# Optimization experiments

Measured on AMD Instinct MI355X. Metric: run time of the kernel, lower is better.

The kernel has to match this reference:

```python
import jax, jax.numpy as jnp
import numpy as np

TOPK = 2


def setup_inputs() -> dict:
    key = jax.random.key(0)
    k1, k2, k3, k4, k5 = jax.random.split(key, 5)
    D, H, E = 1024, 1408, 8
    hidden_states = jax.random.normal(k1, (2, 1024, D), dtype=jnp.float32)
    gate_w = jax.random.normal(k2, (E, D), dtype=jnp.float32) * 0.02
    w1g = jax.random.normal(k3, (E, D, H), dtype=jnp.float32) * 0.02
    w1u = jax.random.normal(k4, (E, D, H), dtype=jnp.float32) * 0.02
    w2 = jax.random.normal(k5, (E, H, D), dtype=jnp.float32) * 0.02
    return {"hidden_states": hidden_states, "gate_w": gate_w, "w1g": w1g, "w1u": w1u, "w2": w2}


def reference(hidden_states, gate_w, w1g, w1u, w2):
    # hidden_states: [B, S, D]; expert weights: w1g/w1u [E, D, H], w2 [E, H, D]
    B, S, D = hidden_states.shape
    E = gate_w.shape[0]
    x = hidden_states.reshape(-1, D)  # [T, D]
    T = x.shape[0]

    # --- MoEGate: softmax scores, top-k routing (no topk renorm) ---
    logits = x @ gate_w.T                      # [T, E]
    scores = jax.nn.softmax(logits, axis=-1)   # [T, E]
    topk_w, topk_idx = jax.lax.top_k(scores, TOPK)  # [T, K]

    # Per-token combine coefficient for each expert: coeff[t, e] = sum_k w[t,k] * (idx[t,k]==e)
    coeff = jnp.zeros((T, E), dtype=x.dtype).at[jnp.arange(T)[:, None], topk_idx].add(topk_w)

    # --- Grouped expert MLP (swiglu): identical math to permute + grouped GEMM + unpermute ---
    g = jnp.einsum('td,edh->teh', x, w1g)      # [T, E, H]
    u = jnp.einsum('td,edh->teh', x, w1u)      # [T, E, H]
    h = jax.nn.silu(g) * u                     # [T, E, H]
    y = jnp.einsum('teh,te,ehd->td', h, coeff, w2)  # [T, D]
    return y.reshape(B, S, D)
```

## Files before the change

### kernel.cpp

```cpp
#include <hip/hip_runtime.h>

#define TOK 2048
#define DDIM 1024
#define HDIM 1408
#define ENUM 8
#define NSLOT (2 * TOK)
#define UP_NB 22
#define UP_KS 32
#define DN_NB 16
#define DN_KS 44

typedef unsigned int uint;
typedef unsigned short ushort;

using bf16x8 = __attribute__((ext_vector_type(8))) __bf16;
using f32x4  = __attribute__((ext_vector_type(4))) float;

__device__ __forceinline__ float silu_f(float g) {
    return g / (1.0f + __expf(-g));
}

__device__ __forceinline__ ushort cvt_bf16(float f) {
    uint u = __float_as_uint(f);
    u += 0x7FFFu + ((u >> 16) & 1u);
    return (ushort)(u >> 16);
}

__device__ __forceinline__ void gl2lds16(const void* g, void* l) {
    __builtin_amdgcn_global_load_lds(
        (const __attribute__((address_space(1))) uint*)g,
        (__attribute__((address_space(3))) uint*)l, 16, 0, 0);
}

__global__ __launch_bounds__(64) void gate1_kernel(
    const float* __restrict__ x, const float* __restrict__ gw,
    int* __restrict__ tinfo, float* __restrict__ wslot, ushort* __restrict__ xb)
{
    const int t = blockIdx.x;
    const int lane = threadIdx.x;
    const float* xr = x + (size_t)t * DDIM;
    ushort* xbr = xb + (size_t)t * DDIM;
    float xv[16];
#pragma unroll
    for (int i = 0; i < 16; ++i) xv[i] = xr[lane + 64 * i];
#pragma unroll
    for (int i = 0; i < 16; ++i) xbr[lane + 64 * i] = cvt_bf16(xv[i]);
    float logit[ENUM];
#pragma unroll
    for (int e = 0; e < ENUM; ++e) {
        const float* gr = gw + (size_t)e * DDIM;
        float acc = 0.f;
#pragma unroll
        for (int i = 0; i < 16; ++i) acc += xv[i] * gr[lane + 64 * i];
#pragma unroll
        for (int s = 32; s > 0; s >>= 1) acc += __shfl_xor(acc, s, 64);
        logit[e] = acc;
    }
    if (lane == 0) {
        float mx = logit[0];
#pragma unroll
        for (int e = 1; e < ENUM; ++e) mx = fmaxf(mx, logit[e]);
        float p[ENUM]; float se = 0.f;
#pragma unroll
        for (int e = 0; e < ENUM; ++e) { p[e] = __expf(logit[e] - mx); se += p[e]; }
        float inv = 1.0f / se;
#pragma unroll
        for (int e = 0; e < ENUM; ++e) p[e] *= inv;
        int i0 = 0;
#pragma unroll
        for (int e = 1; e < ENUM; ++e) if (p[e] > p[i0]) i0 = e;
        int i1 = (i0 == 0) ? 1 : 0;
#pragma unroll
        for (int e = 0; e < ENUM; ++e) if (e != i0 && p[e] > p[i1]) i1 = e;
        tinfo[t] = i0 | (i1 << 4);
        wslot[(t << 1)] = p[i0];
        wslot[(t << 1) | 1] = p[i1];
    }
}

__global__ __launch_bounds__(256) void gate2_kernel(
    const int* __restrict__ tinfo, int* __restrict__ counts, int* __restrict__ toks)
{
    __shared__ int cnt[ENUM];
    const int tid = threadIdx.x;
    if (tid < ENUM) cnt[tid] = 0;
    __syncthreads();
    for (int t = tid; t < TOK; t += 256) {
        int info = tinfo[t];
        int i0 = info & 15, i1 = info >> 4;
        int p0 = atomicAdd(&cnt[i0], 1);
        toks[i0 * TOK + p0] = (t << 1);
        int p1 = atomicAdd(&cnt[i1], 1);
        toks[i1 * TOK + p1] = (t << 1) | 1;
    }
    __syncthreads();
    if (tid < ENUM) counts[tid] = cnt[tid];
}

__device__ __forceinline__ void tcast64_body(
    const float* __restrict__ src, ushort* __restrict__ dst, int N, int KS, int NB,
    int e, int ks, int nb, int tid)
{
    __shared__ float Ls[32][68];
    const float* st = src + (size_t)e * ((size_t)KS * 32) * N + (size_t)(ks * 32) * N + nb * 64;
    const int n4 = (tid & 15) * 4;
#pragma unroll
    for (int r = 0; r < 2; ++r) {
        int k = (tid >> 4) + r * 16;
        float4 v = *(const float4*)(st + (size_t)k * N + n4);
        Ls[k][n4 + 0] = v.x; Ls[k][n4 + 1] = v.y; Ls[k][n4 + 2] = v.z; Ls[k][n4 + 3] = v.w;
    }
    __syncthreads();

    ushort* dt = dst + ((((size_t)e * NB + nb) * KS) + ks) * 2048;
    const int nn = tid >> 2;
    const int kk0 = (tid & 3) * 8;
    ushort o[8];
#pragma unroll
    for (int j = 0; j < 8; ++j) o[j] = cvt_bf16(Ls[kk0 + j][nn]);
    *(uint4*)(dt + nn * 32 + kk0) = *(uint4*)o;
}

__global__ __launch_bounds__(256) void tcast_w1_kernel(
    const float* __restrict__ w1g, const float* __restrict__ w1u,
    ushort* __restrict__ BgP, ushort* __restrict__ BuP)
{
    const int z = blockIdx.z;
    const float* src = (z & 8) ? w1u : w1g;
    ushort* dst = (z & 8) ? BuP : BgP;
    tcast64_body(src, dst, HDIM, UP_KS, UP_NB, z & 7, blockIdx.x, blockIdx.y, threadIdx.x);
}

__global__ __launch_bounds__(256) void tcast_w2_kernel(
    const float* __restrict__ w2, ushort* __restrict__ W2P)
{
    tcast64_body(w2, W2P, DDIM, DN_KS, DN_NB, blockIdx.z, blockIdx.x, blockIdx.y, threadIdx.x);
}

__global__ __launch_bounds__(256, 4) void up_mfma(
    const ushort* __restrict__ xb, const ushort* __restrict__ BgP,
    const ushort* __restrict__ BuP, const int* __restrict__ counts,
    const int* __restrict__ toks, ushort* __restrict__ Hbuf)
{
    const int e = blockIdx.z;
    const int cnt = counts[e];
    const int m0 = blockIdx.y * 64;
    if (m0 >= cnt) return;
    const int nb = blockIdx.x;
    const int tid = threadIdx.x;
    const int w = tid >> 6;
    const int lane = tid & 63;
    const int q = lane >> 4;
    const int l15 = lane & 15;
    const int wr = w >> 1;
    const int wc = w & 1;

    __shared__ ushort As[2][64][32];
    __shared__ ushort Bgs[2][64][32];
    __shared__ ushort Bus[2][64][32];
    __shared__ int rowslot[64];

    if (tid < 64) rowslot[tid] = (m0 + tid < cnt) ? toks[e * TOK + m0 + tid] : -1;
    __syncthreads();

    const int srow = w * 16 + (lane >> 2);
    const int clog = (((lane & 3) + 4 - ((srow >> 1) & 3)) & 3) * 8;
    const int aslot = rowslot[srow];
    const ushort* agp = xb + (size_t)(aslot < 0 ? 0 : (aslot >> 1)) * DDIM + clog;
    const size_t tb = (size_t)(e * UP_NB + nb) * UP_KS * 2048;
    const ushort* bgp = BgP + tb + srow * 32 + clog;
    const ushort* bup = BuP + tb + srow * 32 + clog;

    const int coff = ((q + (l15 >> 1)) & 3) * 8;

    f32x4 accg[2][2], accu[2][2];
#pragma unroll
    for (int i = 0; i < 2; ++i)
#pragma unroll
        for (int j = 0; j < 2; ++j) { accg[i][j] = (f32x4)0.f; accu[i][j] = (f32x4)0.f; }

#define UP_PREFETCH(KSV, B)                                       \
    {                                                             \
        gl2lds16(agp + (KSV) * 32, &As[B][w * 16][0]);            \
        gl2lds16(bgp + (size_t)(KSV) * 2048, &Bgs[B][w * 16][0]); \
        gl2lds16(bup + (size_t)(KSV) * 2048, &Bus[B][w * 16][0]); \
    }

    UP_PREFETCH(0, 0);
    __syncthreads();

    for (int ks = 0; ks < UP_KS; ++ks) {
        const int cur = ks & 1;
        const int nxt = cur ^ 1;
        if (ks + 1 < UP_KS) UP_PREFETCH(ks + 1, nxt);

        bf16x8 a[2], bg[2], bu[2];
#pragma unroll
        for (int mi = 0; mi < 2; ++mi)
            a[mi] = *(const bf16x8*)&As[cur][wr * 32 + mi * 16 + l15][coff];
#pragma unroll
        for (int ni = 0; ni < 2; ++ni) {
            bg[ni] = *(const bf16x8*)&Bgs[cur][wc * 32 + ni * 16 + l15][coff];
            bu[ni] = *(const bf16x8*)&Bus[cur][wc * 32 + ni * 16 + l15][coff];
        }
#pragma unroll
        for (int mi = 0; mi < 2; ++mi)
#pragma unroll
            for (int ni = 0; ni < 2; ++ni) {
                accg[mi][ni] = __builtin_amdgcn_mfma_f32_16x16x32_bf16(a[mi], bg[ni], accg[mi][ni], 0, 0, 0);
                accu[mi][ni] = __builtin_amdgcn_mfma_f32_16x16x32_bf16(a[mi], bu[ni], accu[mi][ni], 0, 0, 0);
            }
        __syncthreads();
    }
#undef UP_PREFETCH

#pragma unroll
    for (int mi = 0; mi < 2; ++mi) {
#pragma unroll
        for (int r = 0; r < 4; ++r) {
            int ml = wr * 32 + mi * 16 + q * 4 + r;
            int slot = rowslot[ml];
            if (slot < 0) continue;
            ushort* hrow = Hbuf + (size_t)slot * HDIM + nb * 64 + wc * 32 + l15;
#pragma unroll
            for (int ni = 0; ni < 2; ++ni)
                hrow[ni * 16] = cvt_bf16(silu_f(accg[mi][ni][r]) * accu[mi][ni][r]);
        }
    }
}

__global__ __launch_bounds__(256, 4) void down_mfma(
    const ushort* __restrict__ Hbuf, const ushort* __restrict__ W2P,
    const int* __restrict__ counts, const int* __restrict__ toks,
    float* __restrict__ Ybuf)
{
    const int e = blockIdx.z;
    const int cnt = counts[e];
    const int m0 = blockIdx.y * 64;
    if (m0 >= cnt) return;
    const int nb = blockIdx.x;
    const int tid = threadIdx.x;
    const int w = tid >> 6;
    const int lane = tid & 63;
    const int q = lane >> 4;
    const int l15 = lane & 15;
    const int wr = w >> 1;
    const int wc = w & 1;

    __shared__ ushort As[2][64][32];
    __shared__ ushort Bs[2][64][32];
    __shared__ int rowslot[64];

    if (tid < 64) rowslot[tid] = (m0 + tid < cnt) ? toks[e * TOK + m0 + tid] : -1;
    __syncthreads();

    const int srow = w * 16 + (lane >> 2);
    const int clog = (((lane & 3) + 4 - ((srow >> 1) & 3)) & 3) * 8;
    const int aslot = rowslot[srow];
    const ushort* agp = Hbuf + (size_t)(aslot < 0 ? 0 : aslot) * HDIM + clog;
    const ushort* bp = W2P + (size_t)(e * DN_NB + nb) * DN_KS * 2048 + srow * 32 + clog;

    const int coff = ((q + (l15 >> 1)) & 3) * 8;

    f32x4 acc[2][2];
#pragma unroll
    for (int i = 0; i < 2; ++i)
#pragma unroll
        for (int j = 0; j < 2; ++j) acc[i][j] = (f32x4)0.f;

#define DN_PREFETCH(KSV, B)                                     \
    {                                                           \
        gl2lds16(agp + (KSV) * 32, &As[B][w * 16][0]);          \
        gl2lds16(bp + (size_t)(KSV) * 2048, &Bs[B][w * 16][0]); \
    }

    DN_PREFETCH(0, 0);
    __syncthreads();

    for (int ks = 0; ks < DN_KS; ++ks) {
        const int cur = ks & 1;
        const int nxt = cur ^ 1;
        if (ks + 1 < DN_KS) DN_PREFETCH(ks + 1, nxt);

        bf16x8 a[2], b[2];
#pragma unroll
        for (int mi = 0; mi < 2; ++mi)
            a[mi] = *(const bf16x8*)&As[cur][wr * 32 + mi * 16 + l15][coff];
#pragma unroll
        for (int ni = 0; ni < 2; ++ni)
            b[ni] = *(const bf16x8*)&Bs[cur][wc * 32 + ni * 16 + l15][coff];
#pragma unroll
        for (int mi = 0; mi < 2; ++mi)
#pragma unroll
            for (int ni = 0; ni < 2; ++ni)
                acc[mi][ni] = __builtin_amdgcn_mfma_f32_16x16x32_bf16(a[mi], b[ni], acc[mi][ni], 0, 0, 0);
        __syncthreads();
    }
#undef DN_PREFETCH

#pragma unroll
    for (int mi = 0; mi < 2; ++mi) {
#pragma unroll
        for (int r = 0; r < 4; ++r) {
            int ml = wr * 32 + mi * 16 + q * 4 + r;
            int slot = rowslot[ml];
            if (slot < 0) continue;
            float* yr = Ybuf + (size_t)slot * DDIM + nb * 64 + wc * 32 + l15;
#pragma unroll
            for (int ni = 0; ni < 2; ++ni)
                yr[ni * 16] = acc[mi][ni][r];
        }
    }
}

__global__ __launch_bounds__(256) void combine_kernel(
    const float* __restrict__ Ybuf, const float* __restrict__ wslot,
    float* __restrict__ y)
{
    const int t = blockIdx.x;
    const int j = threadIdx.x * 4;
    const float w0 = wslot[2 * t];
    const float w1 = wslot[2 * t + 1];
    float4 a = *(const float4*)(Ybuf + ((size_t)2 * t) * DDIM + j);
    float4 b = *(const float4*)(Ybuf + ((size_t)2 * t + 1) * DDIM + j);
    float4 o;
    o.x = w0 * a.x + w1 * b.x;
    o.y = w0 * a.y + w1 * b.y;
    o.z = w0 * a.z + w1 * b.z;
    o.w = w0 * a.w + w1 * b.w;
    *(float4*)(y + (size_t)t * DDIM + j) = o;
}

extern "C" void kernel_launch(void* const* d_in, const int* in_sizes, int n_in,
                              void* d_out, int out_size, void* d_ws, size_t ws_size,
                              hipStream_t stream) {
    const float* x   = (const float*)d_in[0];
    const float* gw  = (const float*)d_in[1];
    const float* w1g = (const float*)d_in[2];
    const float* w1u = (const float*)d_in[3];
    const float* w2  = (const float*)d_in[4];
    float* y = (float*)d_out;
    char* ws = (char*)d_ws;

    size_t off = 0;
    int*    counts = (int*)(ws + off);   off += 256;
    int*    toks   = (int*)(ws + off);   off += (size_t)ENUM * TOK * 4;
    float*  wslot  = (float*)(ws + off); off += (size_t)NSLOT * 4;
    int*    tinfo  = (int*)(ws + off);   off += (size_t)TOK * 4;
    off = (off + 255) & ~(size_t)255;
    ushort* xb     = (ushort*)(ws + off); off += (size_t)TOK * DDIM * 2;
    size_t regA = off;
    ushort* BgP  = (ushort*)(ws + regA);
    ushort* BuP  = (ushort*)(ws + regA + (size_t)ENUM * DDIM * HDIM * 2);
    float*  Ybuf = (float*)(ws + regA);
    off = regA + (size_t)2 * ENUM * DDIM * HDIM * 2;
    ushort* W2P  = (ushort*)(ws + off);  off += (size_t)ENUM * HDIM * DDIM * 2;
    ushort* Hbuf = (ushort*)(ws + off);

    gate1_kernel<<<TOK, 64, 0, stream>>>(x, gw, tinfo, wslot, xb);
    gate2_kernel<<<1, 256, 0, stream>>>(tinfo, counts, toks);

    tcast_w1_kernel<<<dim3(UP_KS, UP_NB, 16), 256, 0, stream>>>(w1g, w1u, BgP, BuP);
    tcast_w2_kernel<<<dim3(DN_KS, DN_NB, ENUM), 256, 0, stream>>>(w2, W2P);

    up_mfma<<<dim3(UP_NB, TOK / 64, ENUM), 256, 0, stream>>>(xb, BgP, BuP, counts, toks, Hbuf);
    down_mfma<<<dim3(DN_NB, TOK / 64, ENUM), 256, 0, stream>>>(Hbuf, W2P, counts, toks, Ybuf);
    combine_kernel<<<TOK, 256, 0, stream>>>(Ybuf, wslot, y);
}
```

Before: 272.0 us.

## Enlarge expert GEMM block tiles from 64x64 to 128x128

Doubles the M and N tile of both grouped expert GEMMs to 128x128, so each wave computes a 64x64 sub-tile with 4x4 MFMA fragments. The weight pre-cast kernels now write 128-column packed panels to match the new layout. Each staged A and B tile feeds more MFMAs, which lowers global and LDS traffic per FLOP. The cost is many more accumulator registers (launch bounds lowered to 2 blocks per SM) and more padded work on expert tiles that are only partly filled.

After: 278.2 us. 1.02x slower.

```diff
diff --git a/kernel.cpp b/kernel.cpp
--- a/kernel.cpp
+++ b/kernel.cpp
@@ -5,9 +5,9 @@
 #define HDIM 1408
 #define ENUM 8
 #define NSLOT (2 * TOK)
-#define UP_NB 22
+#define UP_NB 11
 #define UP_KS 32
-#define DN_NB 16
+#define DN_NB 8
 #define DN_KS 44
 
 typedef unsigned int uint;
@@ -97,28 +97,29 @@
     if (tid < ENUM) counts[tid] = cnt[tid];
 }
 
-__device__ __forceinline__ void tcast64_body(
+__device__ __forceinline__ void tcast128_body(
     const float* __restrict__ src, ushort* __restrict__ dst, int N, int KS, int NB,
     int e, int ks, int nb, int tid)
 {
-    __shared__ float Ls[32][68];
-    const float* st = src + (size_t)e * ((size_t)KS * 32) * N + (size_t)(ks * 32) * N + nb * 64;
-    const int n4 = (tid & 15) * 4;
-#pragma unroll
-    for (int r = 0; r < 2; ++r) {
-        int k = (tid >> 4) + r * 16;
+    __shared__ float Ls[32][132];
+    const float* st = src + (size_t)e * ((size_t)KS * 32) * N + (size_t)(ks * 32) * N + nb * 128;
+    const int n4 = (tid & 31) * 4;
+#pragma unroll
+    for (int r = 0; r < 4; ++r) {
+        int k = (tid >> 5) + r * 8;
         float4 v = *(const float4*)(st + (size_t)k * N + n4);
         Ls[k][n4 + 0] = v.x; Ls[k][n4 + 1] = v.y; Ls[k][n4 + 2] = v.z; Ls[k][n4 + 3] = v.w;
     }
     __syncthreads();
 
-    ushort* dt = dst + ((((size_t)e * NB + nb) * KS) + ks) * 2048;
-    const int nn = tid >> 2;
-    const int kk0 = (tid & 3) * 8;
-    ushort o[8];
-#pragma unroll
-    for (int j = 0; j < 8; ++j) o[j] = cvt_bf16(Ls[kk0 + j][nn]);
-    *(uint4*)(dt + nn * 32 + kk0) = *(uint4*)o;
+    ushort* dt = dst + ((((size_t)e * NB + nb) * KS) + ks) * 4096;
+    const int nn = tid >> 1;
+    const int kk0 = (tid & 1) * 16;
+    ushort o[16];
+#pragma unroll
+    for (int j = 0; j < 16; ++j) o[j] = cvt_bf16(Ls[kk0 + j][nn]);
+    *(uint4*)(dt + nn * 32 + kk0)     = *(uint4*)&o[0];
+    *(uint4*)(dt + nn * 32 + kk0 + 8) = *(uint4*)&o[8];
 }
 
 __global__ __launch_bounds__(256) void tcast_w1_kernel(
@@ -128,23 +129,23 @@
     const int z = blockIdx.z;
     const float* src = (z & 8) ? w1u : w1g;
     ushort* dst = (z & 8) ? BuP : BgP;
-    tcast64_body(src, dst, HDIM, UP_KS, UP_NB, z & 7, blockIdx.x, blockIdx.y, threadIdx.x);
+    tcast128_body(src, dst, HDIM, UP_KS, UP_NB, z & 7, blockIdx.x, blockIdx.y, threadIdx.x);
 }
 
 __global__ __launch_bounds__(256) void tcast_w2_kernel(
     const float* __restrict__ w2, ushort* __restrict__ W2P)
 {
-    tcast64_body(w2, W2P, DDIM, DN_KS, DN_NB, blockIdx.z, blockIdx.x, blockIdx.y, threadIdx.x);
-}
-
-__global__ __launch_bounds__(256, 4) void up_mfma(
+    tcast128_body(w2, W2P, DDIM, DN_KS, DN_NB, blockIdx.z, blockIdx.x, blockIdx.y, threadIdx.x);
+}
+
+__global__ __launch_bounds__(256, 2) void up_mfma(
     const ushort* __restrict__ xb, const ushort* __restrict__ BgP,
     const ushort* __restrict__ BuP, const int* __restrict__ counts,
     const int* __restrict__ toks, ushort* __restrict__ Hbuf)
 {
     const int e = blockIdx.z;
     const int cnt = counts[e];
-    const int m0 = blockIdx.y * 64;
+    const int m0 = blockIdx.y * 128;
     if (m0 >= cnt) return;
     const int nb = blockIdx.x;
     const int tid = threadIdx.x;
@@ -155,35 +156,41 @@
     const int wr = w >> 1;
     const int wc = w & 1;
 
-    __shared__ ushort As[2][64][32];
-    __shared__ ushort Bgs[2][64][32];
-    __shared__ ushort Bus[2][64][32];
-    __shared__ int rowslot[64];
-
-    if (tid < 64) rowslot[tid] = (m0 + tid < cnt) ? toks[e * TOK + m0 + tid] : -1;
-    __syncthreads();
-
-    const int srow = w * 16 + (lane >> 2);
-    const int clog = (((lane & 3) + 4 - ((srow >> 1) & 3)) & 3) * 8;
-    const int aslot = rowslot[srow];
-    const ushort* agp = xb + (size_t)(aslot < 0 ? 0 : (aslot >> 1)) * DDIM + clog;
-    const size_t tb = (size_t)(e * UP_NB + nb) * UP_KS * 2048;
-    const ushort* bgp = BgP + tb + srow * 32 + clog;
-    const ushort* bup = BuP + tb + srow * 32 + clog;
+    __shared__ ushort As[2][128][32];
+    __shared__ ushort Bgs[2][128][32];
+    __shared__ ushort Bus[2][128][32];
+    __shared__ int rowslot[128];
+
+    if (tid < 128) rowslot[tid] = (m0 + tid < cnt) ? toks[e * TOK + m0 + tid] : -1;
+    __syncthreads();
+
+    const int srow0 = w * 32 + (lane >> 2);
+    const int srow1 = srow0 + 16;
+    const int clog = (((lane & 3) + 4 - ((srow0 >> 1) & 3)) & 3) * 8;
+    const int s0 = rowslot[srow0];
+    const int s1 = rowslot[srow1];
+    const ushort* agp0 = xb + (size_t)(s0 < 0 ? 0 : (s0 >> 1)) * DDIM + clog;
+    const ushort* agp1 = xb + (size_t)(s1 < 0 ? 0 : (s1 >> 1)) * DDIM + clog;
+    const size_t tb = (size_t)(e * UP_NB + nb) * UP_KS * 4096;
+    const ushort* bgp = BgP + tb + srow0 * 32 + clog;
+    const ushort* bup = BuP + tb + srow0 * 32 + clog;
 
     const int coff = ((q + (l15 >> 1)) & 3) * 8;
 
-    f32x4 accg[2][2], accu[2][2];
-#pragma unroll
-    for (int i = 0; i < 2; ++i)
-#pragma unroll
-        for (int j = 0; j < 2; ++j) { accg[i][j] = (f32x4)0.f; accu[i][j] = (f32x4)0.f; }
-
-#define UP_PREFETCH(KSV, B)                                       \
-    {                                                             \
-        gl2lds16(agp + (KSV) * 32, &As[B][w * 16][0]);            \
-        gl2lds16(bgp + (size_t)(KSV) * 2048, &Bgs[B][w * 16][0]); \
-        gl2lds16(bup + (size_t)(KSV) * 2048, &Bus[B][w * 16][0]); \
+    f32x4 accg[4][4], accu[4][4];
+#pragma unroll
+    for (int i = 0; i < 4; ++i)
+#pragma unroll
+        for (int j = 0; j < 4; ++j) { accg[i][j] = (f32x4)0.f; accu[i][j] = (f32x4)0.f; }
+
+#define UP_PREFETCH(KSV, B)                                                 \
+    {                                                                       \
+        gl2lds16(agp0 + (KSV) * 32, &As[B][w * 32][0]);                     \
+        gl2lds16(agp1 + (KSV) * 32, &As[B][w * 32 + 16][0]);                \
+        gl2lds16(bgp + (size_t)(KSV) * 4096, &Bgs[B][w * 32][0]);           \
+        gl2lds16(bgp + (size_t)(KSV) * 4096 + 512, &Bgs[B][w * 32 + 16][0]);\
+        gl2lds16(bup + (size_t)(KSV) * 4096, &Bus[B][w * 32][0]);           \
+        gl2lds16(bup + (size_t)(KSV) * 4096 + 512, &Bus[B][w * 32 + 16][0]);\
     }
 
     UP_PREFETCH(0, 0);
@@ -194,19 +201,19 @@
         const int nxt = cur ^ 1;
         if (ks + 1 < UP_KS) UP_PREFETCH(ks + 1, nxt);
 
-        bf16x8 a[2], bg[2], bu[2];
-#pragma unroll
-        for (int mi = 0; mi < 2; ++mi)
-            a[mi] = *(const bf16x8*)&As[cur][wr * 32 + mi * 16 + l15][coff];
-#pragma unroll
-        for (int ni = 0; ni < 2; ++ni) {
-            bg[ni] = *(const bf16x8*)&Bgs[cur][wc * 32 + ni * 16 + l15][coff];
-            bu[ni] = *(const bf16x8*)&Bus[cur][wc * 32 + ni * 16 + l15][coff];
+        bf16x8 a[4], bg[4], bu[4];
+#pragma unroll
+        for (int mi = 0; mi < 4; ++mi)
+            a[mi] = *(const bf16x8*)&As[cur][wr * 64 + mi * 16 + l15][coff];
+#pragma unroll
+        for (int ni = 0; ni < 4; ++ni) {
+            bg[ni] = *(const bf16x8*)&Bgs[cur][wc * 64 + ni * 16 + l15][coff];
+            bu[ni] = *(const bf16x8*)&Bus[cur][wc * 64 + ni * 16 + l15][coff];
         }
 #pragma unroll
-        for (int mi = 0; mi < 2; ++mi)
-#pragma unroll
-            for (int ni = 0; ni < 2; ++ni) {
+        for (int mi = 0; mi < 4; ++mi)
+#pragma unroll
+            for (int ni = 0; ni < 4; ++ni) {
                 accg[mi][ni] = __builtin_amdgcn_mfma_f32_16x16x32_bf16(a[mi], bg[ni], accg[mi][ni], 0, 0, 0);
                 accu[mi][ni] = __builtin_amdgcn_mfma_f32_16x16x32_bf16(a[mi], bu[ni], accu[mi][ni], 0, 0, 0);
             }
@@ -215,28 +222,28 @@
 #undef UP_PREFETCH
 
 #pragma unroll
-    for (int mi = 0; mi < 2; ++mi) {
+    for (int mi = 0; mi < 4; ++mi) {
 #pragma unroll
         for (int r = 0; r < 4; ++r) {
-            int ml = wr * 32 + mi * 16 + q * 4 + r;
+            int ml = wr * 64 + mi * 16 + q * 4 + r;
             int slot = rowslot[ml];
             if (slot < 0) continue;
-            ushort* hrow = Hbuf + (size_t)slot * HDIM + nb * 64 + wc * 32 + l15;
-#pragma unroll
-            for (int ni = 0; ni < 2; ++ni)
+            ushort* hrow = Hbuf + (size_t)slot * HDIM + nb * 128 + wc * 64 + l15;
+#pragma unroll
+            for (int ni = 0; ni < 4; ++ni)
                 hrow[ni * 16] = cvt_bf16(silu_f(accg[mi][ni][r]) * accu[mi][ni][r]);
         }
     }
 }
 
-__global__ __launch_bounds__(256, 4) void down_mfma(
+__global__ __launch_bounds__(256, 2) void down_mfma(
     const ushort* __restrict__ Hbuf, const ushort* __restrict__ W2P,
     const int* __restrict__ counts, const int* __restrict__ toks,
     float* __restrict__ Ybuf)
 {
     const int e = blockIdx.z;
     const int cnt = counts[e];
-    const int m0 = blockIdx.y * 64;
+    const int m0 = blockIdx.y * 128;
     if (m0 >= cnt) return;
     const int nb = blockIdx.x;
     const int tid = threadIdx.x;
@@ -247,31 +254,36 @@
     const int wr = w >> 1;
     const int wc = w & 1;
 
-    __shared__ ushort As[2][64][32];
-    __shared__ ushort Bs[2][64][32];
-    __shared__ int rowslot[64];
-
-    if (tid < 64) rowslot[tid] = (m0 + tid < cnt) ? toks[e * TOK + m0 + tid] : -1;
-    __syncthreads();
-
-    const int srow = w * 16 + (lane >> 2);
-    const int clog = (((lane & 3) + 4 - ((srow >> 1) & 3)) & 3) * 8;
-    const int aslot = rowslot[srow];
-    const ushort* agp = Hbuf + (size_t)(aslot < 0 ? 0 : aslot) * HDIM + clog;
-    const ushort* bp = W2P + (size_t)(e * DN_NB + nb) * DN_KS * 2048 + srow * 32 + clog;
+    __shared__ ushort As[2][128][32];
+    __shared__ ushort Bs[2][128][32];
+    __shared__ int rowslot[128];
+
+    if (tid < 128) rowslot[tid] = (m0 + tid < cnt) ? toks[e * TOK + m0 + tid] : -1;
+    __syncthreads();
+
+    const int srow0 = w * 32 + (lane >> 2);
+    const int srow1 = srow0 + 16;
+    const int clog = (((lane & 3) + 4 - ((srow0 >> 1) & 3)) & 3) * 8;
+    const int s0 = rowslot[srow0];
+    const int s1 = rowslot[srow1];
+    const ushort* agp0 = Hbuf + (size_t)(s0 < 0 ? 0 : s0) * HDIM + clog;
+    const ushort* agp1 = Hbuf + (size_t)(s1 < 0 ? 0 : s1) * HDIM + clog;
+    const ushort* bp = W2P + (size_t)(e * DN_NB + nb) * DN_KS * 4096 + srow0 * 32 + clog;
 
     const int coff = ((q + (l15 >> 1)) & 3) * 8;
 
-    f32x4 acc[2][2];
-#pragma unroll
-    for (int i = 0; i < 2; ++i)
-#pragma unroll
-        for (int j = 0; j < 2; ++j) acc[i][j] = (f32x4)0.f;
-
-#define DN_PREFETCH(KSV, B)                                     \
-    {                                                           \
-        gl2lds16(agp + (KSV) * 32, &As[B][w * 16][0]);          \
-        gl2lds16(bp + (size_t)(KSV) * 2048, &Bs[B][w * 16][0]); \
+    f32x4 acc[4][4];
+#pragma unroll
+    for (int i = 0; i < 4; ++i)
+#pragma unroll
+        for (int j = 0; j < 4; ++j) acc[i][j] = (f32x4)0.f;
+
+#define DN_PREFETCH(KSV, B)                                               \
+    {                                                                     \
+        gl2lds16(agp0 + (KSV) * 32, &As[B][w * 32][0]);                   \
+        gl2lds16(agp1 + (KSV) * 32, &As[B][w * 32 + 16][0]);              \
+        gl2lds16(bp + (size_t)(KSV) * 4096, &Bs[B][w * 32][0]);           \
+        gl2lds16(bp + (size_t)(KSV) * 4096 + 512, &Bs[B][w * 32 + 16][0]);\
     }
 
     DN_PREFETCH(0, 0);
@@ -282,32 +294,32 @@
         const int nxt = cur ^ 1;
         if (ks + 1 < DN_KS) DN_PREFETCH(ks + 1, nxt);
 
-        bf16x8 a[2], b[2];
-#pragma unroll
-        for (int mi = 0; mi < 2; ++mi)
-            a[mi] = *(const bf16x8*)&As[cur][wr * 32 + mi * 16 + l15][coff];
-#pragma unroll
-        for (int ni = 0; ni < 2; ++ni)
-            b[ni] = *(const bf16x8*)&Bs[cur][wc * 32 + ni * 16 + l15][coff];
-#pragma unroll
-        for (int mi = 0; mi < 2; ++mi)
-#pragma unroll
-            for (int ni = 0; ni < 2; ++ni)
+        bf16x8 a[4], b[4];
+#pragma unroll
+        for (int mi = 0; mi < 4; ++mi)
+            a[mi] = *(const bf16x8*)&As[cur][wr * 64 + mi * 16 + l15][coff];
+#pragma unroll
+        for (int ni = 0; ni < 4; ++ni)
+            b[ni] = *(const bf16x8*)&Bs[cur][wc * 64 + ni * 16 + l15][coff];
+#pragma unroll
+        for (int mi = 0; mi < 4; ++mi)
+#pragma unroll
+            for (int ni = 0; ni < 4; ++ni)
                 acc[mi][ni] = __builtin_amdgcn_mfma_f32_16x16x32_bf16(a[mi], b[ni], acc[mi][ni], 0, 0, 0);
         __syncthreads();
     }
 #undef DN_PREFETCH
 
 #pragma unroll
-    for (int mi = 0; mi < 2; ++mi) {
+    for (int mi = 0; mi < 4; ++mi) {
 #pragma unroll
         for (int r = 0; r < 4; ++r) {
-            int ml = wr * 32 + mi * 16 + q * 4 + r;
+            int ml = wr * 64 + mi * 16 + q * 4 + r;
             int slot = rowslot[ml];
             if (slot < 0) continue;
-            float* yr = Ybuf + (size_t)slot * DDIM + nb * 64 + wc * 32 + l15;
-#pragma unroll
-            for (int ni = 0; ni < 2; ++ni)
+            float* yr = Ybuf + (size_t)slot * DDIM + nb * 128 + wc * 64 + l15;
+#pragma unroll
+            for (int ni = 0; ni < 4; ++ni)
                 yr[ni * 16] = acc[mi][ni][r];
         }
     }
@@ -363,7 +375,7 @@
     tcast_w1_kernel<<<dim3(UP_KS, UP_NB, 16), 256, 0, stream>>>(w1g, w1u, BgP, BuP);
     tcast_w2_kernel<<<dim3(DN_KS, DN_NB, ENUM), 256, 0, stream>>>(w2, W2P);
 
-    up_mfma<<<dim3(UP_NB, TOK / 64, ENUM), 256, 0, stream>>>(xb, BgP, BuP, counts, toks, Hbuf);
-    down_mfma<<<dim3(DN_NB, TOK / 64, ENUM), 256, 0, stream>>>(Hbuf, W2P, counts, toks, Ybuf);
+    up_mfma<<<dim3(UP_NB, TOK / 128, ENUM), 256, 0, stream>>>(xb, BgP, BuP, counts, toks, Hbuf);
+    down_mfma<<<dim3(DN_NB, TOK / 128, ENUM), 256, 0, stream>>>(Hbuf, W2P, counts, toks, Ybuf);
     combine_kernel<<<TOK, 256, 0, stream>>>(Ybuf, wslot, y);
 }
```
